# Performance work log

Measured on AMD Instinct MI355X. Metric: run time of the kernel, lower is better.

## Reference

```python
import jax, jax.numpy as jnp
import numpy as np
import jax.lax as lax

EPS = 1e-5

def conv3x3(x, w):
    # x: [B,C,H,W], w: [O,C,3,3], stride 1, padding 1
    return lax.conv_general_dilated(x, w, (1, 1), ((1, 1), (1, 1)),
                                    dimension_numbers=('NCHW', 'OIHW', 'NCHW'))

def bn(x, s, b, m, v):
    inv = s / jnp.sqrt(v + EPS)
    return x * inv[None, :, None, None] + (b - m * inv)[None, :, None, None]

def conv_bn_relu(x, w, s, b, m, v):
    return jax.nn.relu(bn(conv3x3(x, w), s, b, m, v))

def spatial_attention(x, q_w, q_b, v_w, v_b, gamma):
    # Self_attention: q_conv used for both q and k (k_conv is dead in source)
    B, C, H, W = x.shape
    N = H * W
    q = (jnp.einsum('bchw,oc->bohw', x, q_w) + q_b[None, :, None, None]).reshape(B, -1, N)  # [B,Cq,N]
    v = (jnp.einsum('bchw,oc->bohw', x, v_w) + v_b[None, :, None, None]).reshape(B, C, N)   # [B,C,N]
    energy = jnp.einsum('bcn,bcm->bnm', q, q)          # [B,N,N]
    attn = jax.nn.softmax(energy, axis=-1)
    out = jnp.einsum('bcm,bnm->bcn', v, attn)          # v @ attn^T
    return gamma[0] * out.reshape(B, C, H, W) + x

def channel_attention(x, gamma):
    B, C, H, W = x.shape
    xf = x.reshape(B, C, -1)                           # [B,C,N]
    energy = jnp.einsum('bcn,bdn->bcd', xf, xf)        # [B,C,C]
    energy_new = jnp.max(energy, axis=-1, keepdims=True) - energy
    attn = jax.nn.softmax(energy_new, axis=-1)
    out = jnp.einsum('bcd,bdn->bcn', attn, xf)
    return gamma[0] * out.reshape(B, C, H, W) + x

def setup_inputs() -> dict:
    key = jax.random.key(0)
    ks = jax.random.split(key, 32)
    B, Cin, H, W = 4, 512, 64, 64
    Ci, Cq, Cout = 128, 16, 19
    f = jax.random.normal
    u = jax.random.uniform
    d = {}
    d['x'] = f(ks[0], (B, Cin, H, W), jnp.float32)
    d['conv5a_w'] = f(ks[1], (Ci, Cin, 3, 3), jnp.float32) * 0.02
    d['bn5a_s'] = u(ks[2], (Ci,), jnp.float32)
    d['bn5a_b'] = f(ks[3], (Ci,), jnp.float32) * 0.1
    d['bn5a_m'] = f(ks[4], (Ci,), jnp.float32) * 0.1
    d['bn5a_v'] = u(ks[5], (Ci,), jnp.float32) + 0.5
    d['conv5c_w'] = f(ks[6], (Ci, Cin, 3, 3), jnp.float32) * 0.02
    d['bn5c_s'] = u(ks[7], (Ci,), jnp.float32)
    d['bn5c_b'] = f(ks[8], (Ci,), jnp.float32) * 0.1
    d['bn5c_m'] = f(ks[9], (Ci,), jnp.float32) * 0.1
    d['bn5c_v'] = u(ks[10], (Ci,), jnp.float32) + 0.5
    d['q_w'] = f(ks[11], (Cq, Ci), jnp.float32) * 0.05
    d['q_b'] = f(ks[12], (Cq,), jnp.float32) * 0.05
    d['v_w'] = f(ks[13], (Ci, Ci), jnp.float32) * 0.05
    d['v_b'] = f(ks[14], (Ci,), jnp.float32) * 0.05
    d['gamma_sa'] = jnp.zeros((1,), jnp.float32)
    d['gamma_sc'] = jnp.zeros((1,), jnp.float32)
    d['conv51_w'] = f(ks[15], (Ci, Ci, 3, 3), jnp.float32) * 0.03
    d['bn51_s'] = u(ks[16], (Ci,), jnp.float32)
    d['bn51_b'] = f(ks[17], (Ci,), jnp.float32) * 0.1
    d['bn51_m'] = f(ks[18], (Ci,), jnp.float32) * 0.1
    d['bn51_v'] = u(ks[19], (Ci,), jnp.float32) + 0.5
    d['conv52_w'] = f(ks[20], (Ci, Ci, 3, 3), jnp.float32) * 0.03
    d['bn52_s'] = u(ks[21], (Ci,), jnp.float32)
    d['bn52_b'] = f(ks[22], (Ci,), jnp.float32) * 0.1
    d['bn52_m'] = f(ks[23], (Ci,), jnp.float32) * 0.1
    d['bn52_v'] = u(ks[24], (Ci,), jnp.float32) + 0.5
    d['conv8_w'] = f(ks[25], (Cout, Ci), jnp.float32) * 0.05
    d['conv8_b'] = f(ks[26], (Cout,), jnp.float32) * 0.05
    return d

def reference(x, conv5a_w, bn5a_s, bn5a_b, bn5a_m, bn5a_v,
              conv5c_w, bn5c_s, bn5c_b, bn5c_m, bn5c_v,
              q_w, q_b, v_w, v_b, gamma_sa, gamma_sc,
              conv51_w, bn51_s, bn51_b, bn51_m, bn51_v,
              conv52_w, bn52_s, bn52_b, bn52_m, bn52_v,
              conv8_w, conv8_b):
    feat1 = conv_bn_relu(x, conv5a_w, bn5a_s, bn5a_b, bn5a_m, bn5a_v)
    sa_feat = spatial_attention(feat1, q_w, q_b, v_w, v_b, gamma_sa)
    sa_conv = conv_bn_relu(sa_feat, conv51_w, bn51_s, bn51_b, bn51_m, bn51_v)
    feat2 = conv_bn_relu(x, conv5c_w, bn5c_s, bn5c_b, bn5c_m, bn5c_v)
    sc_feat = channel_attention(feat2, gamma_sc)
    sc_conv = conv_bn_relu(sc_feat, conv52_w, bn52_s, bn52_b, bn52_m, bn52_v)
    feat_sum = sa_conv + sc_conv
    # conv8 is a 1x1 conv (Dropout2d is identity in eval mode)
    out = jnp.einsum('bchw,oc->bohw', feat_sum, conv8_w) + conv8_b[None, :, None, None]
    return out
```

## Files before the change

### kernel.cpp

```cpp
#include <hip/hip_runtime.h>
#include <math.h>

#define EPS 1e-5f


typedef unsigned int uint;
typedef unsigned short u16;
typedef u16 u16x4 __attribute__((ext_vector_type(4)));
typedef u16 u16x8 __attribute__((ext_vector_type(8)));
typedef __bf16 bf16x8 __attribute__((ext_vector_type(8)));
typedef float f32x4 __attribute__((ext_vector_type(4)));
typedef float f32x16 __attribute__((ext_vector_type(16)));

#define WAIT_VM16() asm volatile("s_waitcnt vmcnt(16)" ::: "memory")
#define WAIT_VM8()  asm volatile("s_waitcnt vmcnt(8)" ::: "memory")
#define WAIT_VM0()  asm volatile("s_waitcnt vmcnt(0)" ::: "memory")
#define BARRIER()   asm volatile("s_barrier" ::: "memory")

__device__ __forceinline__ u16 f2bf(float f) {
    uint u = __float_as_uint(f);
    u = u + 0x7FFF + ((u >> 16) & 1);
    return (u16)(u >> 16);
}
__device__ __forceinline__ float bf2f(u16 h) {
    return __uint_as_float(((uint)h) << 16);
}

__device__ __forceinline__ void gl_lds16(const void* g, void* l) {
    __builtin_amdgcn_global_load_lds(
        (const __attribute__((address_space(1))) unsigned int*)g,
        (__attribute__((address_space(3))) unsigned int*)l, 16, 0, 0);
}

__global__ void bn_prep_all(const float* s0, const float* b0, const float* m0, const float* v0,
                            const float* s1, const float* b1, const float* m1, const float* v1,
                            const float* s2, const float* b2, const float* m2, const float* v2,
                            const float* s3, const float* b3, const float* m3, const float* v3,
                            float* c0, float* c1, float* c2, float* c3) {
    int k = blockIdx.x, i = threadIdx.x;
    const float *s, *bb, *mm, *vv; float* cf;
    if (k == 0)      { s = s0; bb = b0; mm = m0; vv = v0; cf = c0; }
    else if (k == 1) { s = s1; bb = b1; mm = m1; vv = v1; cf = c1; }
    else if (k == 2) { s = s2; bb = b2; mm = m2; vv = v2; cf = c2; }
    else             { s = s3; bb = b3; mm = m3; vv = v3; cf = c3; }
    float inv = s[i] / sqrtf(vv[i] + EPS);
    cf[i] = inv;
    cf[128 + i] = bb[i] - mm[i] * inv;
}

__global__ void border_zero(u16* x0h, u16* x0l, u16* x1h, u16* x1l, u16* x2h, u16* x2l) {
    int p = blockIdx.x;
    int img = p / 260, pe = p % 260;
    int y, x;
    if (pe < 66)       { y = 0;  x = pe; }
    else if (pe < 132) { y = 65; x = pe - 66; }
    else { int q = pe - 132; y = 1 + (q >> 1); x = (q & 1) * 65; }
    int buf = blockIdx.y, tid = threadIdx.x;
    if (buf == 0) {
        size_t base = (((size_t)img * 66 + y) * 66 + x) * 512;
        for (int c = tid; c < 512; c += 256) { x0h[base + c] = 0; x0l[base + c] = 0; }
    } else {
        u16* hh = (buf == 1) ? x1h : x2h;
        u16* ll = (buf == 1) ? x1l : x2l;
        size_t base = (((size_t)img * 66 + y) * 66 + x) * 128;
        for (int c = tid; c < 128; c += 256) { hh[base + c] = 0; ll[base + c] = 0; }
    }
}

template <int CIN>
__global__ void pack_w(const float* __restrict__ w0, u16* __restrict__ h0, u16* __restrict__ l0,
                       const float* __restrict__ w1, u16* __restrict__ h1, u16* __restrict__ l1) {
    const float* w = blockIdx.z ? w1 : w0;
    u16* hh = blockIdx.z ? h1 : h0;
    u16* ll = blockIdx.z ? l1 : l0;
    int i = blockIdx.x * 256 + threadIdx.x;
    int ic = i & (CIN - 1);
    int rest = i / CIN;
    int oc = rest & 127;
    int tap = rest >> 7;
    float f = w[((size_t)oc * CIN + ic) * 9 + tap];
    u16 h = f2bf(f);
    hh[i] = h;
    ll[i] = f2bf(f - bf2f(h));
}

__global__ void pack_x(const float* __restrict__ x, u16* __restrict__ xh, u16* __restrict__ xl) {
    __shared__ float tile[64][68];
    int cb = blockIdx.x, y = blockIdx.y, b = blockIdx.z, tid = threadIdx.x;
    int cl = tid >> 2, seg = tid & 3;
    const float* src = x + (((size_t)b * 512 + cb * 64 + cl) * 64 + y) * 64 + seg * 16;
#pragma unroll
    for (int j = 0; j < 4; j++)
        *(f32x4*)&tile[cl][seg * 16 + j * 4] = *(const f32x4*)(src + j * 4);
    __syncthreads();
    int pxl = tid >> 2, cg = tid & 3;
    u16x8 h0, h1, l0, l1;
#pragma unroll
    for (int j = 0; j < 8; j++) {
        float v = tile[cg * 16 + j][pxl];
        u16 h = f2bf(v); h0[j] = h; l0[j] = f2bf(v - bf2f(h));
    }
#pragma unroll
    for (int j = 0; j < 8; j++) {
        float v = tile[cg * 16 + 8 + j][pxl];
        u16 h = f2bf(v); h1[j] = h; l1[j] = f2bf(v - bf2f(h));
    }
    size_t dst = (((size_t)b * 66 + y + 1) * 66 + (pxl + 1)) * 512 + cb * 64 + cg * 16;
    *(u16x8*)(xh + dst) = h0;  *(u16x8*)(xh + dst + 8) = h1;
    *(u16x8*)(xl + dst) = l0;  *(u16x8*)(xl + dst + 8) = l1;
}

template <int CIN, bool PACKOUT>
__launch_bounds__(256)
__global__ void conv_mfma(const u16* __restrict__ xh0, const u16* __restrict__ xl0,
                          const u16* __restrict__ xh1, const u16* __restrict__ xl1,
                          const u16* __restrict__ wh0, const u16* __restrict__ wl0,
                          const u16* __restrict__ wh1, const u16* __restrict__ wl1,
                          const float* __restrict__ coef0, const float* __restrict__ coef1,
                          float* __restrict__ fo0, float* __restrict__ fo1,
                          u16* __restrict__ ph0, u16* __restrict__ pl0,
                          u16* __restrict__ ph1, u16* __restrict__ pl1) {
    constexpr int ICC = CIN / 32;
    constexpr int NT  = 9 * ICC;
    const int bid = blockIdx.x;
    const int z  = (bid >> 2) & 1;
    const int b  = bid & 3;
    const int y0 = (bid >> 3) * 2;
    const int tile = b * 32 + (bid >> 3);

    const u16* xh = z ? xh1 : xh0;  const u16* xl = z ? xl1 : xl0;
    const u16* wh = z ? wh1 : wh0;  const u16* wl = z ? wl1 : wl0;
    const float* coef = z ? coef1 : coef0;
    float* fo = z ? fo1 : fo0;
    u16* ph = z ? ph1 : ph0;  u16* pl = z ? pl1 : pl0;

    const int tid = threadIdx.x;

    __shared__ char smem[98304];

    const int cidx = tid & 127;
    const int khv  = (tid >> 7) & 1;
    const u16* bAh = wh + (size_t)cidx * CIN + khv * 8;
    const u16* bAl = wl + (size_t)cidx * CIN + khv * 8;
    const int rr = cidx >> 6, xxc = cidx & 63;
    const size_t rowoff = ((size_t)(b * 66 + y0 + rr) * 66 + xxc) * CIN + khv * 8;
    const u16* bBh = xh + rowoff;
    const u16* bBl = xl + rowoff;
    char* ldst = smem + (tid & 192) * 16;

    const int wid = tid >> 6, lane = tid & 63;
    const int wr = wid >> 1, wc = wid & 1;
    const int l31 = lane & 31, lhi = lane >> 5;
    const int laneA = (lhi * 128 + wr * 64 + l31) * 16;
    const int laneB = 16384 + (lhi * 128 + wc * 64 + l31) * 16;

    f32x16 acc[2][2];
#pragma unroll
    for (int m = 0; m < 2; m++)
#pragma unroll
        for (int n = 0; n < 2; n++)
#pragma unroll
            for (int r = 0; r < 16; r++) acc[m][n][r] = 0.0f;

    auto stage = [&](int t, int buf) {
        const int tap = t / ICC;
        const int ic0 = (t % ICC) * 32;
        const int offA = tap * 128 * CIN + ic0;
        const int offB = ((tap / 3) * 66 + (tap % 3)) * CIN + ic0;
        char* ld = ldst + buf * 32768;
        gl_lds16(bAh + offA,      ld);
        gl_lds16(bAh + offA + 16, ld + 4096);
        gl_lds16(bAl + offA,      ld + 8192);
        gl_lds16(bAl + offA + 16, ld + 12288);
        gl_lds16(bBh + offB,      ld + 16384);
        gl_lds16(bBh + offB + 16, ld + 20480);
        gl_lds16(bBl + offB,      ld + 24576);
        gl_lds16(bBl + offB + 16, ld + 28672);
    };

    stage(0, 0);
    stage(1, 1);

    int buf = 0;
    int hb  = 2;
    for (int t = 0; t < NT; ++t) {
        if (t + 2 < NT) {
            stage(t + 2, hb);
            WAIT_VM16();
        } else if (t + 1 < NT) {
            WAIT_VM8();
        } else {
            WAIT_VM0();
        }
        BARRIER();

        const char* sb = smem + buf * 32768;

        bf16x8 Ah[2][2], Al[2][2], Bh[2][2], Bl[2][2];
#pragma unroll
        for (int kk = 0; kk < 2; kk++)
#pragma unroll
            for (int m = 0; m < 2; m++) {
                Ah[m][kk] = *(const bf16x8*)(sb + laneA + kk * 4096 + m * 512);
                Al[m][kk] = *(const bf16x8*)(sb + 8192 + laneA + kk * 4096 + m * 512);
            }
#pragma unroll
        for (int kk = 0; kk < 2; kk++)
#pragma unroll
            for (int n = 0; n < 2; n++) {
                Bh[n][kk] = *(const bf16x8*)(sb + laneB + kk * 4096 + n * 512);
                Bl[n][kk] = *(const bf16x8*)(sb + 8192 + laneB + kk * 4096 + n * 512);
            }
        __builtin_amdgcn_s_setprio(1);
#pragma unroll
        for (int m = 0; m < 2; m++)
#pragma unroll
            for (int n = 0; n < 2; n++)
#pragma unroll
                for (int kk = 0; kk < 2; kk++) {
                    acc[m][n] = __builtin_amdgcn_mfma_f32_32x32x16_bf16(Ah[m][kk], Bh[n][kk], acc[m][n], 0, 0, 0);
                    acc[m][n] = __builtin_amdgcn_mfma_f32_32x32x16_bf16(Ah[m][kk], Bl[n][kk], acc[m][n], 0, 0, 0);
                    acc[m][n] = __builtin_amdgcn_mfma_f32_32x32x16_bf16(Al[m][kk], Bh[n][kk], acc[m][n], 0, 0, 0);
                }
        __builtin_amdgcn_s_setprio(0);
        BARRIER();

        buf = buf + 1; if (buf == 3) buf = 0;
        hb  = hb + 1;  if (hb == 3)  hb = 0;
    }

#pragma unroll
    for (int n = 0; n < 2; n++) {
        const int pxl = wc * 64 + n * 32 + l31;
        const int pxg = tile * 128 + pxl;
        const int bb = pxg >> 12, yy = (pxg >> 6) & 63, xg = pxg & 63;
        const size_t fbase = (size_t)pxg * 128;
        const size_t pbase = (((size_t)bb * 66 + yy + 1) * 66 + (xg + 1)) * 128;
#pragma unroll
        for (int m = 0; m < 2; m++)
#pragma unroll
            for (int q = 0; q < 4; q++) {
                const int oc4 = wr * 64 + m * 32 + q * 8 + lhi * 4;
                f32x4 sc = *(const f32x4*)&coef[oc4];
                f32x4 sh = *(const f32x4*)&coef[128 + oc4];
                f32x4 outv;
                u16x4 hv, lv;
#pragma unroll
                for (int j = 0; j < 4; j++) {
                    float v = acc[m][n][q * 4 + j] * sc[j] + sh[j];
                    v = v > 0.0f ? v : 0.0f;
                    outv[j] = v;
                    if (PACKOUT) {
                        u16 h = f2bf(v);
                        hv[j] = h;
                        lv[j] = f2bf(v - bf2f(h));
                    }
                }
                *(f32x4*)&fo[fbase + oc4] = outv;
                if (PACKOUT) {
                    *(u16x4*)&ph[pbase + oc4] = hv;
                    *(u16x4*)&pl[pbase + oc4] = lv;
                }
            }
    }
}

__launch_bounds__(256)
__global__ void conv1x1(const float* __restrict__ fa, const float* __restrict__ fb,
                        const float* __restrict__ w8, const float* __restrict__ b8,
                        float* __restrict__ out) {
    __shared__ float s_w[128 * 20];
    int tid = threadIdx.x;
    for (int i = tid; i < 19 * 128; i += 256) {
        int o = i >> 7, c = i & 127;
        s_w[c * 20 + o] = w8[i];
    }
    __syncthreads();
    size_t px = (size_t)blockIdx.x * 256 + tid;
    const f32x4* A = (const f32x4*)(fa + px * 128);
    const f32x4* B = (const f32x4*)(fb + px * 128);
    float acc[19];
#pragma unroll
    for (int o = 0; o < 19; o++) acc[o] = 0.0f;
    for (int cq = 0; cq < 32; cq++) {
        f32x4 v = A[cq] + B[cq];
#pragma unroll
        for (int j = 0; j < 4; j++) {
            float iv = v[j];
            int c = cq * 4 + j;
#pragma unroll
            for (int o = 0; o < 19; o++) acc[o] += iv * s_w[c * 20 + o];
        }
    }
    int b = px >> 12, n = px & 4095;
#pragma unroll
    for (int o = 0; o < 19; o++)
        out[((size_t)b * 19 + o) * 4096 + n] = acc[o] + b8[o];
}


__global__ void lin_q(const float* __restrict__ g, const float* __restrict__ feat,
                      const float* __restrict__ qw, const float* __restrict__ qb,
                      float* __restrict__ outq) {
    if (g[0] == 0.0f) return;
    __shared__ float s_w[16 * 128];
    int tid = threadIdx.x;
    for (int i = tid; i < 2048; i += 256) s_w[i] = qw[i];
    __syncthreads();
    size_t px = (size_t)blockIdx.x * 256 + tid;
    const float* in = feat + px * 128;
    float acc[16];
#pragma unroll
    for (int o = 0; o < 16; o++) acc[o] = 0.0f;
    for (int c = 0; c < 128; c++) {
        float iv = in[c];
#pragma unroll
        for (int o = 0; o < 16; o++) acc[o] += iv * s_w[o * 128 + c];
    }
#pragma unroll
    for (int o = 0; o < 16; o++) outq[px * 16 + o] = acc[o] + qb[o];
}

__global__ void lin_v(const float* __restrict__ g, const float* __restrict__ feat,
                      const float* __restrict__ vw, const float* __restrict__ vb,
                      float* __restrict__ outv) {
    if (g[0] == 0.0f) return;
    int tid = threadIdx.x;
    size_t px = (size_t)blockIdx.x * 64 + (tid >> 2);
    int q4 = tid & 3;
    const float* in = feat + px * 128;
    float acc[32];
#pragma unroll
    for (int j = 0; j < 32; j++) acc[j] = 0.0f;
    for (int c = 0; c < 128; c++) {
        float iv = in[c];
        for (int j = 0; j < 32; j++) acc[j] += iv * vw[(size_t)(q4 * 32 + j) * 128 + c];
    }
    for (int j = 0; j < 32; j++)
        outv[px * 128 + q4 * 32 + j] = acc[j] + vb[q4 * 32 + j];
}

__global__ void sa_attn(const float* __restrict__ g, const float* __restrict__ qb,
                        const float* __restrict__ vb, const float* __restrict__ feat1,
                        u16* __restrict__ ph, u16* __restrict__ pl) {
    if (g[0] == 0.0f) return;
    float gamma = g[0];
    int b = blockIdx.y, grp = blockIdx.x, tid = threadIdx.x;
    __shared__ float s_e[4096];
    __shared__ float s_red[256];
    __shared__ float s_q[16];
    __shared__ float s_o[256];
    for (int ni = 0; ni < 32; ni++) {
        int n = grp * 32 + ni;
        if (tid < 16) s_q[tid] = qb[((size_t)b * 4096 + n) * 16 + tid];
        __syncthreads();
        float lmax = -1e30f;
        for (int m = tid; m < 4096; m += 256) {
            const float* qm = qb + ((size_t)b * 4096 + m) * 16;
            float e = 0.0f;
#pragma unroll
            for (int k = 0; k < 16; k++) e += s_q[k] * qm[k];
            s_e[m] = e;
            lmax = fmaxf(lmax, e);
        }
        s_red[tid] = lmax;
        __syncthreads();
        for (int s = 128; s > 0; s >>= 1) {
            if (tid < s) s_red[tid] = fmaxf(s_red[tid], s_red[tid + s]);
            __syncthreads();
        }
        float mx = s_red[0];
        __syncthreads();
        float lsum = 0.0f;
        for (int m = tid; m < 4096; m += 256) {
            float p = expf(s_e[m] - mx);
            s_e[m] = p;
            lsum += p;
        }
        s_red[tid] = lsum;
        __syncthreads();
        for (int s = 128; s > 0; s >>= 1) {
            if (tid < s) s_red[tid] += s_red[tid + s];
            __syncthreads();
        }
        float denom = s_red[0];
        __syncthreads();
        int c = tid & 127, half = tid >> 7;
        float acc = 0.0f;
        for (int m = half * 2048; m < half * 2048 + 2048; m++)
            acc += s_e[m] * vb[((size_t)b * 4096 + m) * 128 + c];
        s_o[tid] = acc;
        __syncthreads();
        if (tid < 128) {
            float o = (s_o[tid] + s_o[tid + 128]) / denom;
            float val = feat1[((size_t)b * 4096 + n) * 128 + tid] + gamma * o;
            int yy = n >> 6, xx = n & 63;
            size_t pidx = (((size_t)b * 66 + yy + 1) * 66 + (xx + 1)) * 128 + tid;
            u16 h = f2bf(val);
            ph[pidx] = h;
            pl[pidx] = f2bf(val - bf2f(h));
        }
        __syncthreads();
    }
}

__global__ void ca_attn(const float* __restrict__ g, const float* __restrict__ feat2,
                        u16* __restrict__ ph, u16* __restrict__ pl) {
    if (g[0] == 0.0f) return;
    float gamma = g[0];
    int b = blockIdx.y, crow = blockIdx.x, d = threadIdx.x;
    __shared__ float s_red[128];
    __shared__ float s_attn[128];
    const float* base = feat2 + (size_t)b * 4096 * 128;
    float e = 0.0f;
    for (int n = 0; n < 4096; n++) e += base[(size_t)n * 128 + crow] * base[(size_t)n * 128 + d];
    s_red[d] = e;
    __syncthreads();
    for (int s = 64; s > 0; s >>= 1) {
        if (d < s) s_red[d] = fmaxf(s_red[d], s_red[d + s]);
        __syncthreads();
    }
    float m1 = s_red[0];
    __syncthreads();
    float en = m1 - e;
    s_red[d] = en;
    __syncthreads();
    for (int s = 64; s > 0; s >>= 1) {
        if (d < s) s_red[d] = fmaxf(s_red[d], s_red[d + s]);
        __syncthreads();
    }
    float m2 = s_red[0];
    __syncthreads();
    float p = expf(en - m2);
    s_red[d] = p;
    __syncthreads();
    for (int s = 64; s > 0; s >>= 1) {
        if (d < s) s_red[d] += s_red[d + s];
        __syncthreads();
    }
    s_attn[d] = p / s_red[0];
    __syncthreads();
    for (int n = d; n < 4096; n += 128) {
        float acc = 0.0f;
#pragma unroll 8
        for (int dd = 0; dd < 128; dd++) acc += s_attn[dd] * base[(size_t)n * 128 + dd];
        float val = base[(size_t)n * 128 + crow] + gamma * acc;
        int yy = n >> 6, xx = n & 63;
        size_t pidx = (((size_t)b * 66 + yy + 1) * 66 + (xx + 1)) * 128 + crow;
        u16 h = f2bf(val);
        ph[pidx] = h;
        pl[pidx] = f2bf(val - bf2f(h));
    }
}

extern "C" void kernel_launch(void* const* d_in, const int* in_sizes, int n_in,
                              void* d_out, int out_size, void* d_ws, size_t ws_size,
                              hipStream_t stream) {
    const float* x      = (const float*)d_in[0];
    const float* w5a    = (const float*)d_in[1];
    const float* bn5a_s = (const float*)d_in[2];
    const float* bn5a_b = (const float*)d_in[3];
    const float* bn5a_m = (const float*)d_in[4];
    const float* bn5a_v = (const float*)d_in[5];
    const float* w5c    = (const float*)d_in[6];
    const float* bn5c_s = (const float*)d_in[7];
    const float* bn5c_b = (const float*)d_in[8];
    const float* bn5c_m = (const float*)d_in[9];
    const float* bn5c_v = (const float*)d_in[10];
    const float* q_w    = (const float*)d_in[11];
    const float* q_b    = (const float*)d_in[12];
    const float* v_w    = (const float*)d_in[13];
    const float* v_b    = (const float*)d_in[14];
    const float* g_sa   = (const float*)d_in[15];
    const float* g_sc   = (const float*)d_in[16];
    const float* w51    = (const float*)d_in[17];
    const float* bn51_s = (const float*)d_in[18];
    const float* bn51_b = (const float*)d_in[19];
    const float* bn51_m = (const float*)d_in[20];
    const float* bn51_v = (const float*)d_in[21];
    const float* w52    = (const float*)d_in[22];
    const float* bn52_s = (const float*)d_in[23];
    const float* bn52_b = (const float*)d_in[24];
    const float* bn52_m = (const float*)d_in[25];
    const float* bn52_v = (const float*)d_in[26];
    const float* w8     = (const float*)d_in[27];
    const float* b8     = (const float*)d_in[28];
    float* out = (float*)d_out;
    (void)in_sizes; (void)n_in; (void)out_size; (void)ws_size;

    char* W = (char*)d_ws;
    constexpr size_t XP0 = (size_t)4 * 66 * 66 * 512 * 2;
    constexpr size_t XP1 = (size_t)4 * 66 * 66 * 128 * 2;
    constexpr size_t WPA = (size_t)9 * 128 * 512 * 2;
    constexpr size_t WPB = (size_t)9 * 128 * 128 * 2;
    constexpr size_t FT  = (size_t)4 * 4096 * 128 * 4;
    size_t off = 0;
    u16* xp0h = (u16*)(W + off); off += XP0;
    u16* xp0l = (u16*)(W + off); off += XP0;
    u16* xp1h = (u16*)(W + off); off += XP1;
    u16* xp1l = (u16*)(W + off); off += XP1;
    u16* xp2h = (u16*)(W + off); off += XP1;
    u16* xp2l = (u16*)(W + off); off += XP1;
    u16* wp5ah = (u16*)(W + off); off += WPA;
    u16* wp5al = (u16*)(W + off); off += WPA;
    u16* wp5ch = (u16*)(W + off); off += WPA;
    u16* wp5cl = (u16*)(W + off); off += WPA;
    u16* wp51h = (u16*)(W + off); off += WPB;
    u16* wp51l = (u16*)(W + off); off += WPB;
    u16* wp52h = (u16*)(W + off); off += WPB;
    u16* wp52l = (u16*)(W + off); off += WPB;
    float* c5a = (float*)(W + off); off += 1024;
    float* c5c = (float*)(W + off); off += 1024;
    float* c51 = (float*)(W + off); off += 1024;
    float* c52 = (float*)(W + off); off += 1024;
    float* b0  = (float*)(W + off); off += FT;
    float* b1  = (float*)(W + off); off += FT;
    float* b3a = (float*)(W + off); off += FT;
    float* b3b = (float*)(W + off); off += FT;
    float* qbuf = b3a;
    float* vbuf = (float*)((char*)b3a + 1048576);

    border_zero<<<dim3(1040, 3), 256, 0, stream>>>(xp0h, xp0l, xp1h, xp1l, xp2h, xp2l);
    bn_prep_all<<<4, 128, 0, stream>>>(bn5a_s, bn5a_b, bn5a_m, bn5a_v,
                                       bn5c_s, bn5c_b, bn5c_m, bn5c_v,
                                       bn51_s, bn51_b, bn51_m, bn51_v,
                                       bn52_s, bn52_b, bn52_m, bn52_v,
                                       c5a, c5c, c51, c52);
    pack_w<512><<<dim3(2304, 1, 2), 256, 0, stream>>>(w5a, wp5ah, wp5al, w5c, wp5ch, wp5cl);
    pack_w<128><<<dim3(576, 1, 2), 256, 0, stream>>>(w51, wp51h, wp51l, w52, wp52h, wp52l);
    pack_x<<<dim3(8, 64, 4), 256, 0, stream>>>(x, xp0h, xp0l);

    conv_mfma<512, true><<<256, 256, 0, stream>>>(
        xp0h, xp0l, xp0h, xp0l,
        wp5ah, wp5al, wp5ch, wp5cl,
        c5a, c5c, b0, b1,
        xp1h, xp1l, xp2h, xp2l);

    lin_q<<<64, 256, 0, stream>>>(g_sa, b0, q_w, q_b, qbuf);
    lin_v<<<256, 256, 0, stream>>>(g_sa, b0, v_w, v_b, vbuf);
    sa_attn<<<dim3(128, 4), 256, 0, stream>>>(g_sa, qbuf, vbuf, b0, xp1h, xp1l);
    ca_attn<<<dim3(128, 4), 128, 0, stream>>>(g_sc, b1, xp2h, xp2l);

    conv_mfma<128, false><<<256, 256, 0, stream>>>(
        xp1h, xp1l, xp2h, xp2l,
        wp51h, wp51l, wp52h, wp52l,
        c51, c52, b3a, b3b,
        nullptr, nullptr, nullptr, nullptr);

    conv1x1<<<64, 256, 0, stream>>>(b3a, b3b, w8, b8, out);
}
```

Before: 380.0 us.

## Halve conv pixel tile to one row per block, doubling grid to 512

The MFMA conv kernel now computes a 128-channel by 64-pixel tile (one image row) per block instead of two rows, and the grid doubles from 256 to 512 blocks. On a GPU with 256 CUs, 256 blocks fill each CU with only one block, so this adds parallelism and cuts LDS use per block, which lets more blocks reside per CU. In exchange each block reuses the weight tile across half as many pixels, so weight traffic per output doubles and each wave's MFMA-to-load ratio drops.

```diff
diff --git a/kernel.cpp b/kernel.cpp
--- a/kernel.cpp
+++ b/kernel.cpp
@@ -12,8 +12,8 @@
 typedef float f32x4 __attribute__((ext_vector_type(4)));
 typedef float f32x16 __attribute__((ext_vector_type(16)));
 
-#define WAIT_VM16() asm volatile("s_waitcnt vmcnt(16)" ::: "memory")
-#define WAIT_VM8()  asm volatile("s_waitcnt vmcnt(8)" ::: "memory")
+#define WAIT_VM12() asm volatile("s_waitcnt vmcnt(12)" ::: "memory")
+#define WAIT_VM6()  asm volatile("s_waitcnt vmcnt(6)" ::: "memory")
 #define WAIT_VM0()  asm volatile("s_waitcnt vmcnt(0)" ::: "memory")
 #define BARRIER()   asm volatile("s_barrier" ::: "memory")
 
@@ -125,8 +125,7 @@
     const int bid = blockIdx.x;
     const int z  = (bid >> 2) & 1;
     const int b  = bid & 3;
-    const int y0 = (bid >> 3) * 2;
-    const int tile = b * 32 + (bid >> 3);
+    const int y0 = bid >> 3;
 
     const u16* xh = z ? xh1 : xh0;  const u16* xl = z ? xl1 : xl0;
     const u16* wh = z ? wh1 : wh0;  const u16* wl = z ? wl1 : wl0;
@@ -136,46 +135,43 @@
 
     const int tid = threadIdx.x;
 
-    __shared__ char smem[98304];
-
-    const int cidx = tid & 127;
-    const int khv  = (tid >> 7) & 1;
-    const u16* bAh = wh + (size_t)cidx * CIN + khv * 8;
-    const u16* bAl = wl + (size_t)cidx * CIN + khv * 8;
-    const int rr = cidx >> 6, xxc = cidx & 63;
-    const size_t rowoff = ((size_t)(b * 66 + y0 + rr) * 66 + xxc) * CIN + khv * 8;
-    const u16* bBh = xh + rowoff;
-    const u16* bBl = xl + rowoff;
+    __shared__ char smem[73728];
+
+    const int aRow = tid & 127;
+    const int aKh  = tid >> 7;
+    const u16* bAh = wh + (size_t)aRow * CIN + aKh * 8;
+    const u16* bAl = wl + (size_t)aRow * CIN + aKh * 8;
+    const int bPx = tid & 63;
+    const size_t rowbase = ((size_t)(b * 66 + y0) * 66 + bPx) * CIN
+                         + ((tid >> 6) & 1) * 8 + (tid >> 7) * 16;
+    const u16* bBh = xh + rowbase;
+    const u16* bBl = xl + rowbase;
     char* ldst = smem + (tid & 192) * 16;
 
     const int wid = tid >> 6, lane = tid & 63;
     const int wr = wid >> 1, wc = wid & 1;
     const int l31 = lane & 31, lhi = lane >> 5;
-    const int laneA = (lhi * 128 + wr * 64 + l31) * 16;
-    const int laneB = 16384 + (lhi * 128 + wc * 64 + l31) * 16;
-
-    f32x16 acc[2][2];
+    const int laneA = lhi * 2048 + (wr * 64 + l31) * 16;
+    const int laneB = 16384 + lhi * 1024 + (wc * 32 + l31) * 16;
+
+    f32x16 acc[2];
 #pragma unroll
     for (int m = 0; m < 2; m++)
 #pragma unroll
-        for (int n = 0; n < 2; n++)
-#pragma unroll
-            for (int r = 0; r < 16; r++) acc[m][n][r] = 0.0f;
+        for (int r = 0; r < 16; r++) acc[m][r] = 0.0f;
 
     auto stage = [&](int t, int buf) {
         const int tap = t / ICC;
         const int ic0 = (t % ICC) * 32;
         const int offA = tap * 128 * CIN + ic0;
         const int offB = ((tap / 3) * 66 + (tap % 3)) * CIN + ic0;
-        char* ld = ldst + buf * 32768;
+        char* ld = ldst + buf * 24576;
         gl_lds16(bAh + offA,      ld);
         gl_lds16(bAh + offA + 16, ld + 4096);
         gl_lds16(bAl + offA,      ld + 8192);
         gl_lds16(bAl + offA + 16, ld + 12288);
         gl_lds16(bBh + offB,      ld + 16384);
-        gl_lds16(bBh + offB + 16, ld + 20480);
-        gl_lds16(bBl + offB,      ld + 24576);
-        gl_lds16(bBl + offB + 16, ld + 28672);
+        gl_lds16(bBl + offB,      ld + 20480);
     };
 
     stage(0, 0);
@@ -186,42 +182,38 @@
     for (int t = 0; t < NT; ++t) {
         if (t + 2 < NT) {
             stage(t + 2, hb);
-            WAIT_VM16();
+            WAIT_VM12();
         } else if (t + 1 < NT) {
-            WAIT_VM8();
+            WAIT_VM6();
         } else {
             WAIT_VM0();
         }
         BARRIER();
 
-        const char* sb = smem + buf * 32768;
-
-        bf16x8 Ah[2][2], Al[2][2], Bh[2][2], Bl[2][2];
+        const char* sb = smem + buf * 24576;
+
+        bf16x8 Ah[2][2], Al[2][2], Bh[2], Bl[2];
 #pragma unroll
         for (int kk = 0; kk < 2; kk++)
 #pragma unroll
             for (int m = 0; m < 2; m++) {
-                Ah[m][kk] = *(const bf16x8*)(sb + laneA + kk * 4096 + m * 512);
-                Al[m][kk] = *(const bf16x8*)(sb + 8192 + laneA + kk * 4096 + m * 512);
+                Ah[m][kk] = *(const bf16x8*)(sb + kk * 4096 + laneA + m * 512);
+                Al[m][kk] = *(const bf16x8*)(sb + 8192 + kk * 4096 + laneA + m * 512);
             }
 #pragma unroll
-        for (int kk = 0; kk < 2; kk++)
-#pragma unroll
-            for (int n = 0; n < 2; n++) {
-                Bh[n][kk] = *(const bf16x8*)(sb + laneB + kk * 4096 + n * 512);
-                Bl[n][kk] = *(const bf16x8*)(sb + 8192 + laneB + kk * 4096 + n * 512);
+        for (int kk = 0; kk < 2; kk++) {
+            Bh[kk] = *(const bf16x8*)(sb + laneB + kk * 2048);
+            Bl[kk] = *(const bf16x8*)(sb + laneB + 4096 + kk * 2048);
+        }
+        __builtin_amdgcn_s_setprio(1);
+#pragma unroll
+        for (int m = 0; m < 2; m++)
+#pragma unroll
+            for (int kk = 0; kk < 2; kk++) {
+                acc[m] = __builtin_amdgcn_mfma_f32_32x32x16_bf16(Ah[m][kk], Bh[kk], acc[m], 0, 0, 0);
+                acc[m] = __builtin_amdgcn_mfma_f32_32x32x16_bf16(Ah[m][kk], Bl[kk], acc[m], 0, 0, 0);
+                acc[m] = __builtin_amdgcn_mfma_f32_32x32x16_bf16(Al[m][kk], Bh[kk], acc[m], 0, 0, 0);
             }
-        __builtin_amdgcn_s_setprio(1);
-#pragma unroll
-        for (int m = 0; m < 2; m++)
-#pragma unroll
-            for (int n = 0; n < 2; n++)
-#pragma unroll
-                for (int kk = 0; kk < 2; kk++) {
-                    acc[m][n] = __builtin_amdgcn_mfma_f32_32x32x16_bf16(Ah[m][kk], Bh[n][kk], acc[m][n], 0, 0, 0);
-                    acc[m][n] = __builtin_amdgcn_mfma_f32_32x32x16_bf16(Ah[m][kk], Bl[n][kk], acc[m][n], 0, 0, 0);
-                    acc[m][n] = __builtin_amdgcn_mfma_f32_32x32x16_bf16(Al[m][kk], Bh[n][kk], acc[m][n], 0, 0, 0);
-                }
         __builtin_amdgcn_s_setprio(0);
         BARRIER();
 
@@ -229,40 +221,36 @@
         hb  = hb + 1;  if (hb == 3)  hb = 0;
     }
 
-#pragma unroll
-    for (int n = 0; n < 2; n++) {
-        const int pxl = wc * 64 + n * 32 + l31;
-        const int pxg = tile * 128 + pxl;
-        const int bb = pxg >> 12, yy = (pxg >> 6) & 63, xg = pxg & 63;
-        const size_t fbase = (size_t)pxg * 128;
-        const size_t pbase = (((size_t)bb * 66 + yy + 1) * 66 + (xg + 1)) * 128;
-#pragma unroll
-        for (int m = 0; m < 2; m++)
-#pragma unroll
-            for (int q = 0; q < 4; q++) {
-                const int oc4 = wr * 64 + m * 32 + q * 8 + lhi * 4;
-                f32x4 sc = *(const f32x4*)&coef[oc4];
-                f32x4 sh = *(const f32x4*)&coef[128 + oc4];
-                f32x4 outv;
-                u16x4 hv, lv;
-#pragma unroll
-                for (int j = 0; j < 4; j++) {
-                    float v = acc[m][n][q * 4 + j] * sc[j] + sh[j];
-                    v = v > 0.0f ? v : 0.0f;
-                    outv[j] = v;
-                    if (PACKOUT) {
-                        u16 h = f2bf(v);
-                        hv[j] = h;
-                        lv[j] = f2bf(v - bf2f(h));
-                    }
-                }
-                *(f32x4*)&fo[fbase + oc4] = outv;
+    const int col = wc * 32 + l31;
+    const int pxg = b * 4096 + y0 * 64 + col;
+    const size_t fbase = (size_t)pxg * 128;
+    const size_t pbase = (((size_t)b * 66 + y0 + 1) * 66 + (col + 1)) * 128;
+#pragma unroll
+    for (int m = 0; m < 2; m++)
+#pragma unroll
+        for (int q = 0; q < 4; q++) {
+            const int oc4 = wr * 64 + m * 32 + q * 8 + lhi * 4;
+            f32x4 sc = *(const f32x4*)&coef[oc4];
+            f32x4 sh = *(const f32x4*)&coef[128 + oc4];
+            f32x4 outv;
+            u16x4 hv, lv;
+#pragma unroll
+            for (int j = 0; j < 4; j++) {
+                float v = acc[m][q * 4 + j] * sc[j] + sh[j];
+                v = v > 0.0f ? v : 0.0f;
+                outv[j] = v;
                 if (PACKOUT) {
-                    *(u16x4*)&ph[pbase + oc4] = hv;
-                    *(u16x4*)&pl[pbase + oc4] = lv;
+                    u16 h = f2bf(v);
+                    hv[j] = h;
+                    lv[j] = f2bf(v - bf2f(h));
                 }
             }
-    }
+            *(f32x4*)&fo[fbase + oc4] = outv;
+            if (PACKOUT) {
+                *(u16x4*)&ph[pbase + oc4] = hv;
+                *(u16x4*)&pl[pbase + oc4] = lv;
+            }
+        }
 }
 
 __launch_bounds__(256)
@@ -530,7 +518,7 @@
     pack_w<128><<<dim3(576, 1, 2), 256, 0, stream>>>(w51, wp51h, wp51l, w52, wp52h, wp52l);
     pack_x<<<dim3(8, 64, 4), 256, 0, stream>>>(x, xp0h, xp0l);
 
-    conv_mfma<512, true><<<256, 256, 0, stream>>>(
+    conv_mfma<512, true><<<512, 256, 0, stream>>>(
         xp0h, xp0l, xp0h, xp0l,
         wp5ah, wp5al, wp5ch, wp5cl,
         c5a, c5c, b0, b1,
@@ -541,7 +529,7 @@
     sa_attn<<<dim3(128, 4), 256, 0, stream>>>(g_sa, qbuf, vbuf, b0, xp1h, xp1l);
     ca_attn<<<dim3(128, 4), 128, 0, stream>>>(g_sc, b1, xp2h, xp2l);
 
-    conv_mfma<128, false><<<256, 256, 0, stream>>>(
+    conv_mfma<128, false><<<512, 256, 0, stream>>>(
         xp1h, xp1l, xp2h, xp2l,
         wp51h, wp51l, wp52h, wp52l,
         c51, c52, b3a, b3b,
```

Result: slower. 447.9 us (+17.9%).
